# Kernel tuning notes

Hardware: AMD Instinct MI355X
Metric: run time of the kernel (lower is better)

## Reference

```python
import jax, jax.numpy as jnp
import numpy as np

DIM_EMB = 1024
NUM_HEADS = 16
DIM_HEAD = DIM_EMB // NUM_HEADS  # 64


def setup_inputs() -> dict:
    key = jax.random.key(0)
    k1, k2, k3 = jax.random.split(key, 3)
    x = jax.random.normal(k1, (4, 2048, DIM_EMB), dtype=jnp.float32)
    # nn.Linear(dim_embedding, 3*h*d, bias=False): weight shape [out, in]
    w_qkv = jax.random.normal(k2, (3 * NUM_HEADS * DIM_HEAD, DIM_EMB), dtype=jnp.float32) * (DIM_EMB ** -0.5)
    w_out = jax.random.normal(k3, (DIM_EMB, NUM_HEADS * DIM_HEAD), dtype=jnp.float32) * ((NUM_HEADS * DIM_HEAD) ** -0.5)
    return {"x": x, "w_qkv": w_qkv, "w_out": w_out}


def reference(x, w_qkv, w_out):
    b, t, _ = x.shape
    scale = DIM_HEAD ** -0.5
    qkv = jnp.einsum('bte,fe->btf', x, w_qkv)  # [b, t, 3*h*d]
    qkv = qkv.reshape(b, t, 3, NUM_HEADS, DIM_HEAD)  # fused dim order (k h d)
    q, k, v = qkv[:, :, 0], qkv[:, :, 1], qkv[:, :, 2]  # each [b, t, h, d]
    scores = jnp.einsum('bihd,bjhd->bhij', q, k) * scale  # [b, h, t, t]
    weights = jax.nn.softmax(scores, axis=-1)
    attn = jnp.einsum('bhij,bjhd->bhid', weights, v)  # [b, h, t, d]
    concat = attn.transpose(0, 2, 1, 3).reshape(b, t, NUM_HEADS * DIM_HEAD)
    return jnp.einsum('btf,ef->bte', concat, w_out)
```

## Files before the change

kernel.cpp:

```cpp
#include <hip/hip_runtime.h>

#define DI __device__ __forceinline__

typedef float  f32x2  __attribute__((ext_vector_type(2)));
typedef float  f32x4  __attribute__((ext_vector_type(4)));
typedef float  f32x16 __attribute__((ext_vector_type(16)));
typedef __bf16 bf16x8 __attribute__((ext_vector_type(8)));
typedef unsigned u32x2 __attribute__((ext_vector_type(2)));
typedef unsigned u32x4 __attribute__((ext_vector_type(4)));

static constexpr int TB   = 2048;
static constexpr int NTOK = 8192;
static constexpr int EMB  = 1024;
static constexpr int FQKV = 3072;

DI unsigned short f2bf(float f) {
  union { float f; unsigned u; } v; v.f = f;
  unsigned r = v.u + 0x7FFFu + ((v.u >> 16) & 1u);
  return (unsigned short)(r >> 16);
}

DI unsigned pack2bf(float a, float b) {
#if __has_builtin(__builtin_amdgcn_cvt_pk_bf16_f32)
  typedef __bf16 bf16x2 __attribute__((ext_vector_type(2)));
  bf16x2 r = __builtin_amdgcn_cvt_pk_bf16_f32(a, b);
  return __builtin_bit_cast(unsigned, r);
#else
  unsigned ua = __builtin_bit_cast(unsigned, a) + 0x8000u;
  unsigned ub = __builtin_bit_cast(unsigned, b) + 0x8000u;
  return __builtin_amdgcn_perm(ub, ua, 0x07060302u);
#endif
}

DI void plswap(unsigned& a, unsigned& b) {
#if __has_builtin(__builtin_amdgcn_permlane32_swap)
  u32x2 r = __builtin_amdgcn_permlane32_swap(a, b, false, false);
  a = r.x; b = r.y;
#else
  const bool hi = (threadIdx.x & 32) != 0;
  unsigned ax = (unsigned)__shfl_xor((int)a, 32);
  unsigned bx = (unsigned)__shfl_xor((int)b, 32);
  unsigned na = hi ? bx : a;
  unsigned nb = hi ? b : ax;
  a = na; b = nb;
#endif
}

DI bf16x8 frag4(unsigned a, unsigned b, unsigned c, unsigned d) {
  u32x4 u = {a, b, c, d};
  return __builtin_bit_cast(bf16x8, u);
}

DI void gload16(const void* g, void* l) {
  __builtin_amdgcn_global_load_lds(
      (__attribute__((address_space(1))) void*)(g),
      (__attribute__((address_space(3))) void*)(l), 16, 0, 0);
}

DI void syncdrain() {
  __builtin_amdgcn_s_waitcnt(0);
  __syncthreads();
}

__global__ __launch_bounds__(256)
void cvt_kernel(const float4* __restrict__ x, const float4* __restrict__ wq,
                const float4* __restrict__ wo,
                ushort4* __restrict__ xb, ushort4* __restrict__ wqb,
                ushort4* __restrict__ wob) {
  const int i  = blockIdx.x * 256 + threadIdx.x;
  const int nx = NTOK * EMB / 4;
  const int nq = FQKV * EMB / 4;
  float4 v; ushort4* dst;
  if (i < nx)           { v = x[i];           dst = xb  + i; }
  else if (i < nx + nq) { v = wq[i - nx];     dst = wqb + (i - nx); }
  else                  { v = wo[i - nx - nq]; dst = wob + (i - nx - nq); }
  ushort4 p;
  p.x = f2bf(v.x); p.y = f2bf(v.y); p.z = f2bf(v.z); p.w = f2bf(v.w);
  *dst = p;
}

template <int MODE>
__global__ __launch_bounds__(256)
void gemm_bt(const unsigned short* __restrict__ A,
             const unsigned short* __restrict__ Bt,
             const int K,
             unsigned short* __restrict__ qk,
             unsigned short* __restrict__ vT,
             float* __restrict__ outp) {
  __shared__ unsigned short sA[128 * 32];
  __shared__ unsigned short sB[128 * 32];
  const int tid  = threadIdx.x;
  const int w    = tid >> 6;
  const int l    = tid & 63;
  const int quad = l >> 4;
  const int lr   = l & 15;
  const int n0   = blockIdx.x * 128;
  const int m0   = blockIdx.y * 128;
  const int wm   = (w >> 1) * 64;
  const int wn   = (w & 1) * 64;

  f32x4 acc[4][4];
#pragma unroll
  for (int i = 0; i < 4; ++i)
#pragma unroll
    for (int j = 0; j < 4; ++j) acc[i][j] = {0.f, 0.f, 0.f, 0.f};

  const int srow = l >> 2;
  const int sg   = (l & 3) ^ ((l >> 3) & 3);
  const unsigned short* gA = A  + (long)(m0 + w * 32 + srow) * K + sg * 8;
  const unsigned short* gB = Bt + (long)(n0 + w * 32 + srow) * K + sg * 8;
  unsigned short* lA = sA + w * 1024;
  unsigned short* lB = sB + w * 1024;
  const int swz = (lr >> 1) & 3;

  for (int k0 = 0; k0 < K; k0 += 32) {
    gload16(gA + k0,          lA);
    gload16(gA + k0 + 16 * K, lA + 512);
    gload16(gB + k0,          lB);
    gload16(gB + k0 + 16 * K, lB + 512);
    syncdrain();
    bf16x8 af[4], bfr[4];
#pragma unroll
    for (int rt = 0; rt < 4; ++rt)
      af[rt] = *(const bf16x8*)(sA + (wm + rt * 16 + lr) * 32 + (quad ^ swz) * 8);
#pragma unroll
    for (int ct = 0; ct < 4; ++ct)
      bfr[ct] = *(const bf16x8*)(sB + (wn + ct * 16 + lr) * 32 + (quad ^ swz) * 8);
#pragma unroll
    for (int rt = 0; rt < 4; ++rt)
#pragma unroll
      for (int ct = 0; ct < 4; ++ct)
        acc[rt][ct] = __builtin_amdgcn_mfma_f32_16x16x32_bf16(af[rt], bfr[ct],
                                                              acc[rt][ct], 0, 0, 0);
    __syncthreads();
  }

  if (MODE == 0) {
    if (n0 < 2048) {
      const float qs = (n0 < 1024) ? 0.18033688011112042f : 1.0f;
#pragma unroll
      for (int rt = 0; rt < 4; ++rt) {
        const int row = m0 + wm + rt * 16 + quad * 4;
#pragma unroll
        for (int ct = 0; ct < 4; ++ct) {
          const int col = n0 + wn + ct * 16 + lr;
#pragma unroll
          for (int r = 0; r < 4; ++r)
            qk[(long)(row + r) * 2048 + col] = f2bf(acc[rt][ct][r] * qs);
        }
      }
    } else {
#pragma unroll
      for (int rt = 0; rt < 4; ++rt) {
        const int tok = m0 + wm + rt * 16 + quad * 4;
        const int bb  = tok >> 11, tt = tok & 2047;
#pragma unroll
        for (int ct = 0; ct < 4; ++ct) {
          const int fv = n0 - 2048 + wn + ct * 16 + lr;
          ushort4 p;
          p.x = f2bf(acc[rt][ct][0]); p.y = f2bf(acc[rt][ct][1]);
          p.z = f2bf(acc[rt][ct][2]); p.w = f2bf(acc[rt][ct][3]);
          *(ushort4*)(vT + ((long)(bb * 1024 + fv)) * 2048 + tt) = p;
        }
      }
    }
  } else {
#pragma unroll
    for (int rt = 0; rt < 4; ++rt) {
      const int row = m0 + wm + rt * 16 + quad * 4;
#pragma unroll
      for (int ct = 0; ct < 4; ++ct) {
        const int col = n0 + wn + ct * 16 + lr;
#pragma unroll
        for (int r = 0; r < 4; ++r)
          outp[(long)(row + r) * 1024 + col] = acc[rt][ct][r];
      }
    }
  }
}

__global__ __launch_bounds__(256, 4)
void attn_kernel(const unsigned short* __restrict__ qk,
                 const unsigned short* __restrict__ vT,
                 unsigned short* __restrict__ attnb) {
  __shared__ unsigned short sK[2][64 * 64];
  __shared__ unsigned short sV[2][64 * 64];
  const int tid = threadIdx.x;
  const int w   = tid >> 6;
  const int l   = tid & 63;
  const int l31 = l & 31;
  const int lh  = l >> 5;
  const int h8  = lh * 8;
  const int bh  = blockIdx.x;
  const int hh  = bh & 15;
  const long tokbase = (long)(bh >> 4) * TB;
  const int qbase = blockIdx.y * 128 + w * 32;

  bf16x8 qf[4];
  {
    const unsigned short* qptr = qk + (tokbase + qbase + l31) * 2048 + hh * 64 + h8;
#pragma unroll
    for (int s = 0; s < 4; ++s) qf[s] = *(const bf16x8*)(qptr + s * 16);
  }

  const int srow = l >> 3;
  const int g    = (l & 7) ^ srow;
  const unsigned short* kbase =
      qk + (tokbase + w * 16 + srow) * 2048 + 1024 + hh * 64 + g * 8;
  const unsigned short* vbase =
      vT + ((long)bh * 64 + w * 16 + srow) * 2048 + g * 8;

  f32x16 oacc[2] = {{}, {}};
  f32x2 lp2 = {0.f, 0.f};

  gload16(kbase,            &sK[0][(w * 16 + 0) * 64]);
  gload16(kbase + 8 * 2048, &sK[0][(w * 16 + 8) * 64]);
  gload16(vbase,            &sV[0][(w * 16 + 0) * 64]);
  gload16(vbase + 8 * 2048, &sV[0][(w * 16 + 8) * 64]);
  syncdrain();

  for (int t = 0; t < 32; ++t) {
    const int buf = t & 1;
    if (t + 1 < 32) {
      const int k0 = (t + 1) * 64;
      const int nb = buf ^ 1;
      gload16(kbase + (long)k0 * 2048,            &sK[nb][(w * 16 + 0) * 64]);
      gload16(kbase + (long)k0 * 2048 + 8 * 2048, &sK[nb][(w * 16 + 8) * 64]);
      gload16(vbase + k0,                         &sV[nb][(w * 16 + 0) * 64]);
      gload16(vbase + k0 + 8 * 2048,              &sV[nb][(w * 16 + 8) * 64]);
    }
    const unsigned short* bK = sK[buf];
    const unsigned short* bV = sV[buf];

#pragma unroll
    for (int G = 0; G < 2; ++G) {
      f32x16 sacc = {};
      __builtin_amdgcn_s_setprio(1);
#pragma unroll
      for (int s = 0; s < 4; ++s) {
        const int key = G * 32 + l31;
        const int p   = (s * 2 + lh) ^ (key & 7);
        const bf16x8 kf = *(const bf16x8*)(bK + key * 64 + p * 8);
        sacc = __builtin_amdgcn_mfma_f32_32x32x16_bf16(kf, qf[s], sacc, 0, 0, 0);
      }
      __builtin_amdgcn_s_setprio(0);
      float e[16];
#pragma unroll
      for (int i = 0; i < 16; ++i) e[i] = __builtin_amdgcn_exp2f(sacc[i]);
#pragma unroll
      for (int i = 0; i < 8; ++i) {
        f32x2 pr = {e[2 * i], e[2 * i + 1]};
        lp2 += pr;
      }
      unsigned d[8];
#pragma unroll
      for (int i = 0; i < 8; ++i) d[i] = pack2bf(e[2 * i], e[2 * i + 1]);
      plswap(d[0], d[2]); plswap(d[1], d[3]);
      plswap(d[4], d[6]); plswap(d[5], d[7]);
      bf16x8 pp[2];
      pp[0] = frag4(d[0], d[1], d[2], d[3]);
      pp[1] = frag4(d[4], d[5], d[6], d[7]);
      __builtin_amdgcn_s_setprio(1);
#pragma unroll
      for (int sub = 0; sub < 2; ++sub) {
        const int gt  = (G * 2 + sub) * 2 + lh;
        const int d0r = l31, d1r = 32 + l31;
        const bf16x8 vf0 = *(const bf16x8*)(bV + d0r * 64 + ((gt ^ (d0r & 7))) * 8);
        const bf16x8 vf1 = *(const bf16x8*)(bV + d1r * 64 + ((gt ^ (d1r & 7))) * 8);
        oacc[0] = __builtin_amdgcn_mfma_f32_32x32x16_bf16(pp[sub], vf0, oacc[0], 0, 0, 0);
        oacc[1] = __builtin_amdgcn_mfma_f32_32x32x16_bf16(pp[sub], vf1, oacc[1], 0, 0, 0);
      }
      __builtin_amdgcn_s_setprio(0);
    }
    syncdrain();
  }

  const float lp = lp2.x + lp2.y;
  const float fs = lp + __shfl_xor(lp, 32);
  const float rc = 1.0f / fs;
#pragma unroll
  for (int r = 0; r < 16; ++r) {
    const int row = (r & 3) + 8 * (r >> 2) + 4 * lh;
    const float sc = __shfl(rc, row);
    const long base = (tokbase + qbase + row) * 1024 + hh * 64;
    attnb[base + l31]      = f2bf(oacc[0][r] * sc);
    attnb[base + 32 + l31] = f2bf(oacc[1][r] * sc);
  }
}

extern "C" void kernel_launch(void* const* d_in, const int* in_sizes, int n_in,
                              void* d_out, int out_size, void* d_ws, size_t ws_size,
                              hipStream_t stream) {
  const float* x    = (const float*)d_in[0];
  const float* wqkv = (const float*)d_in[1];
  const float* wout = (const float*)d_in[2];
  float* outp = (float*)d_out;

  unsigned short* xb    = (unsigned short*)d_ws;
  unsigned short* wqkvb = xb    + (long)NTOK * EMB;
  unsigned short* woutb = wqkvb + (long)FQKV * EMB;
  unsigned short* qkb   = woutb + (long)EMB * EMB;
  unsigned short* vTb   = qkb   + (long)NTOK * 2048;
  unsigned short* attnb = vTb   + (long)4 * 16 * 64 * TB;

  cvt_kernel<<<12288, 256, 0, stream>>>(
      (const float4*)x, (const float4*)wqkv, (const float4*)wout,
      (ushort4*)xb, (ushort4*)wqkvb, (ushort4*)woutb);

  gemm_bt<0><<<dim3(24, 64), 256, 0, stream>>>(xb, wqkvb, EMB, qkb, vTb, nullptr);

  attn_kernel<<<dim3(64, 16), 256, 0, stream>>>(qkb, vTb, attnb);

  gemm_bt<1><<<dim3(8, 64), 256, 0, stream>>>(attnb, woutb, EMB, nullptr, nullptr, outp);
}
```

Measured before the change: 274.2 us.

## Use 256x256 double-buffered QKV GEMM and double-buffer output GEMM with block swizzle

Replaces the 128x128 QKV projection GEMM with a new 512-thread kernel using 256x256 tiles, a K-step of 64, double-buffered LDS and an XOR-swizzled layout. The generic GEMM also gets double-buffered LDS so global loads for the next K-tile overlap MFMA work on the current one. Both GEMMs remap block indices so neighbouring workgroups share input tiles in cache. The larger tile raises data reuse and cuts LDS traffic per flop, at the cost of heavy register and LDS use (128 KB LDS per block), which limits occupancy.

Measured after the change: 276.5 us. Within noise of the previous version (+0.8%).

```diff
diff --git a/kernel.cpp b/kernel.cpp
--- a/kernel.cpp
+++ b/kernel.cpp
@@ -79,6 +79,109 @@
   *dst = p;
 }
 
+__global__ __launch_bounds__(512, 2)
+void gemm256(const unsigned short* __restrict__ A,
+             const unsigned short* __restrict__ Bt,
+             const int K,
+             unsigned short* __restrict__ qk,
+             unsigned short* __restrict__ vT) {
+  __shared__ unsigned short sA[2][256 * 64];
+  __shared__ unsigned short sB[2][256 * 64];
+  const int tid  = threadIdx.x;
+  const int w    = tid >> 6;
+  const int l    = tid & 63;
+  const int quad = l >> 4;
+  const int lr   = l & 15;
+  const int nwg  = gridDim.x * gridDim.y;
+  const int orig = blockIdx.y * gridDim.x + blockIdx.x;
+  const int swz  = (orig & 7) * (nwg >> 3) + (orig >> 3);
+  const int n0   = (swz % gridDim.x) * 256;
+  const int m0   = (swz / gridDim.x) * 256;
+  const int wm   = (w >> 2) * 128;
+  const int wn   = (w & 3) * 64;
+
+  f32x4 acc[8][4];
+#pragma unroll
+  for (int i = 0; i < 8; ++i)
+#pragma unroll
+    for (int j = 0; j < 4; ++j) acc[i][j] = {0.f, 0.f, 0.f, 0.f};
+
+  const int srow8 = l >> 3;
+  const int gsw   = ((l & 7) ^ srow8) * 8;
+  const unsigned short* gA0 = A  + (long)(m0 + w * 8 + srow8) * K + gsw;
+  const unsigned short* gB0 = Bt + (long)(n0 + w * 8 + srow8) * K + gsw;
+
+  const int NT = K >> 6;
+
+#define STAGE256(buf, kk)                                                      \
+  do {                                                                         \
+    _Pragma("unroll")                                                          \
+    for (int jj = 0; jj < 4; ++jj) {                                           \
+      gload16(gA0 + (long)jj * 64 * K + (kk), &sA[buf][(jj * 64 + w * 8) * 64]);\
+      gload16(gB0 + (long)jj * 64 * K + (kk), &sB[buf][(jj * 64 + w * 8) * 64]);\
+    }                                                                          \
+  } while (0)
+
+  STAGE256(0, 0);
+  syncdrain();
+
+  for (int t = 0; t < NT; ++t) {
+    const int cur = t & 1;
+    if (t + 1 < NT) STAGE256(cur ^ 1, (t + 1) * 64);
+    const unsigned short* aS = &sA[cur][0];
+    const unsigned short* bS = &sB[cur][0];
+#pragma unroll
+    for (int ks = 0; ks < 2; ++ks) {
+      bf16x8 bfr[4];
+#pragma unroll
+      for (int nf = 0; nf < 4; ++nf) {
+        const int r = wn + nf * 16 + lr;
+        bfr[nf] = *(const bf16x8*)(bS + r * 64 + ((ks * 4 + quad) ^ (r & 7)) * 8);
+      }
+#pragma unroll
+      for (int m = 0; m < 8; ++m) {
+        const int ra = wm + m * 16 + lr;
+        const bf16x8 af = *(const bf16x8*)(aS + ra * 64 + ((ks * 4 + quad) ^ (ra & 7)) * 8);
+#pragma unroll
+        for (int nf = 0; nf < 4; ++nf)
+          acc[m][nf] = __builtin_amdgcn_mfma_f32_16x16x32_bf16(af, bfr[nf],
+                                                               acc[m][nf], 0, 0, 0);
+      }
+    }
+    syncdrain();
+  }
+#undef STAGE256
+
+  if (n0 < 2048) {
+    const float qs = (n0 < 1024) ? 0.18033688011112042f : 1.0f;
+#pragma unroll
+    for (int m = 0; m < 8; ++m) {
+      const int row = m0 + wm + m * 16 + quad * 4;
+#pragma unroll
+      for (int nf = 0; nf < 4; ++nf) {
+        const int col = n0 + wn + nf * 16 + lr;
+#pragma unroll
+        for (int r = 0; r < 4; ++r)
+          qk[(long)(row + r) * 2048 + col] = f2bf(acc[m][nf][r] * qs);
+      }
+    }
+  } else {
+#pragma unroll
+    for (int m = 0; m < 8; ++m) {
+      const int tok = m0 + wm + m * 16 + quad * 4;
+      const int bb  = tok >> 11, tt = tok & 2047;
+#pragma unroll
+      for (int nf = 0; nf < 4; ++nf) {
+        const int fv = n0 - 2048 + wn + nf * 16 + lr;
+        ushort4 p;
+        p.x = f2bf(acc[m][nf][0]); p.y = f2bf(acc[m][nf][1]);
+        p.z = f2bf(acc[m][nf][2]); p.w = f2bf(acc[m][nf][3]);
+        *(ushort4*)(vT + ((long)(bb * 1024 + fv)) * 2048 + tt) = p;
+      }
+    }
+  }
+}
+
 template <int MODE>
 __global__ __launch_bounds__(256)
 void gemm_bt(const unsigned short* __restrict__ A,
@@ -87,15 +190,18 @@
              unsigned short* __restrict__ qk,
              unsigned short* __restrict__ vT,
              float* __restrict__ outp) {
-  __shared__ unsigned short sA[128 * 32];
-  __shared__ unsigned short sB[128 * 32];
+  __shared__ unsigned short sA[2][128 * 32];
+  __shared__ unsigned short sB[2][128 * 32];
   const int tid  = threadIdx.x;
   const int w    = tid >> 6;
   const int l    = tid & 63;
   const int quad = l >> 4;
   const int lr   = l & 15;
-  const int n0   = blockIdx.x * 128;
-  const int m0   = blockIdx.y * 128;
+  const int nwg  = gridDim.x * gridDim.y;
+  const int orig = blockIdx.y * gridDim.x + blockIdx.x;
+  const int swzb = (orig & 7) * (nwg >> 3) + (orig >> 3);
+  const int n0   = (swzb % gridDim.x) * 128;
+  const int m0   = (swzb / gridDim.x) * 128;
   const int wm   = (w >> 1) * 64;
   const int wn   = (w & 1) * 64;
 
@@ -109,30 +215,39 @@
   const int sg   = (l & 3) ^ ((l >> 3) & 3);
   const unsigned short* gA = A  + (long)(m0 + w * 32 + srow) * K + sg * 8;
   const unsigned short* gB = Bt + (long)(n0 + w * 32 + srow) * K + sg * 8;
-  unsigned short* lA = sA + w * 1024;
-  unsigned short* lB = sB + w * 1024;
-  const int swz = (lr >> 1) & 3;
-
-  for (int k0 = 0; k0 < K; k0 += 32) {
-    gload16(gA + k0,          lA);
-    gload16(gA + k0 + 16 * K, lA + 512);
-    gload16(gB + k0,          lB);
-    gload16(gB + k0 + 16 * K, lB + 512);
-    syncdrain();
+  const int lofs = w * 1024;
+  const int swz  = (lr >> 1) & 3;
+  const int NT   = K >> 5;
+
+  gload16(gA,          &sA[0][lofs]);
+  gload16(gA + 16 * K, &sA[0][lofs + 512]);
+  gload16(gB,          &sB[0][lofs]);
+  gload16(gB + 16 * K, &sB[0][lofs + 512]);
+  syncdrain();
+
+  for (int t = 0; t < NT; ++t) {
+    const int cur = t & 1;
+    if (t + 1 < NT) {
+      const int k0 = (t + 1) * 32;
+      gload16(gA + k0,          &sA[cur ^ 1][lofs]);
+      gload16(gA + k0 + 16 * K, &sA[cur ^ 1][lofs + 512]);
+      gload16(gB + k0,          &sB[cur ^ 1][lofs]);
+      gload16(gB + k0 + 16 * K, &sB[cur ^ 1][lofs + 512]);
+    }
     bf16x8 af[4], bfr[4];
 #pragma unroll
     for (int rt = 0; rt < 4; ++rt)
-      af[rt] = *(const bf16x8*)(sA + (wm + rt * 16 + lr) * 32 + (quad ^ swz) * 8);
+      af[rt] = *(const bf16x8*)(&sA[cur][(wm + rt * 16 + lr) * 32 + (quad ^ swz) * 8]);
 #pragma unroll
     for (int ct = 0; ct < 4; ++ct)
-      bfr[ct] = *(const bf16x8*)(sB + (wn + ct * 16 + lr) * 32 + (quad ^ swz) * 8);
+      bfr[ct] = *(const bf16x8*)(&sB[cur][(wn + ct * 16 + lr) * 32 + (quad ^ swz) * 8]);
 #pragma unroll
     for (int rt = 0; rt < 4; ++rt)
 #pragma unroll
       for (int ct = 0; ct < 4; ++ct)
         acc[rt][ct] = __builtin_amdgcn_mfma_f32_16x16x32_bf16(af[rt], bfr[ct],
                                                               acc[rt][ct], 0, 0, 0);
-    __syncthreads();
+    syncdrain();
   }
 
   if (MODE == 0) {
@@ -307,7 +422,7 @@
       (const float4*)x, (const float4*)wqkv, (const float4*)wout,
       (ushort4*)xb, (ushort4*)wqkvb, (ushort4*)woutb);
 
-  gemm_bt<0><<<dim3(24, 64), 256, 0, stream>>>(xb, wqkvb, EMB, qkb, vTb, nullptr);
+  gemm256<<<dim3(12, 32), 512, 0, stream>>>(xb, wqkvb, EMB, qkb, vTb);
 
   attn_kernel<<<dim3(64, 16), 256, 0, stream>>>(qkb, vTb, attnb);
 
```

## Replace GEMMs with 256x256 double-buffered 8-wave pipelined kernel; relax attention waits

Applied to the files above, without the earlier changes.

The QKV and output-projection GEMMs now use a 256x256 tile with 8 waves, a K-step of 64 and double-buffered LDS. Global-to-LDS loads are staged across four compute phases with counted vmcnt waits instead of a full drain each iteration. A block-index swizzle is added to improve L2 locality. The attention kernel replaces its full waitcnt(0)+syncthreads with vmcnt(4) waits and raw barriers so the next tile's prefetch can stay in flight. The risks are lower occupancy from the larger LDS footprint, fewer workgroups for the output GEMM (128 blocks), and correctness depending on the hand-counted waits.

New measurement: 287.6 us. +4.9%, slower.

```diff
diff --git a/kernel.cpp b/kernel.cpp
--- a/kernel.cpp
+++ b/kernel.cpp
@@ -56,6 +56,11 @@
       (__attribute__((address_space(1))) void*)(g),
       (__attribute__((address_space(3))) void*)(l), 16, 0, 0);
 }
+
+DI void wait_vm4() { asm volatile("s_waitcnt vmcnt(4)" ::: "memory"); }
+DI void wait_vm0() { asm volatile("s_waitcnt vmcnt(0)" ::: "memory"); }
+DI void rbar()     { __builtin_amdgcn_s_barrier(); }
+DI void sfence()   { __builtin_amdgcn_sched_barrier(0); }
 
 DI void syncdrain() {
   __builtin_amdgcn_s_waitcnt(0);
@@ -80,100 +85,169 @@
 }
 
 template <int MODE>
-__global__ __launch_bounds__(256)
-void gemm_bt(const unsigned short* __restrict__ A,
-             const unsigned short* __restrict__ Bt,
-             const int K,
-             unsigned short* __restrict__ qk,
-             unsigned short* __restrict__ vT,
-             float* __restrict__ outp) {
-  __shared__ unsigned short sA[128 * 32];
-  __shared__ unsigned short sB[128 * 32];
+__global__ __launch_bounds__(512, 2)
+void gemm8p(const unsigned short* __restrict__ A,
+            const unsigned short* __restrict__ Bt,
+            const int K,
+            unsigned short* __restrict__ qk,
+            unsigned short* __restrict__ vT,
+            float* __restrict__ outp) {
+  __shared__ unsigned short sA[2][256 * 64];
+  __shared__ unsigned short sB[2][256 * 64];
   const int tid  = threadIdx.x;
   const int w    = tid >> 6;
   const int l    = tid & 63;
   const int quad = l >> 4;
   const int lr   = l & 15;
-  const int n0   = blockIdx.x * 128;
-  const int m0   = blockIdx.y * 128;
-  const int wm   = (w >> 1) * 64;
-  const int wn   = (w & 1) * 64;
-
-  f32x4 acc[4][4];
-#pragma unroll
-  for (int i = 0; i < 4; ++i)
+  const int nwg  = gridDim.x * gridDim.y;
+  const int orig = blockIdx.y * gridDim.x + blockIdx.x;
+  const int swz  = (orig & 7) * (nwg >> 3) + (orig >> 3);
+  const int n0   = (swz % gridDim.x) * 256;
+  const int m0   = (swz / gridDim.x) * 256;
+  const int wm   = (w >> 2) * 128;
+  const int wn   = (w & 3) * 64;
+
+  f32x4 acc[8][4];
+#pragma unroll
+  for (int i = 0; i < 8; ++i)
 #pragma unroll
     for (int j = 0; j < 4; ++j) acc[i][j] = {0.f, 0.f, 0.f, 0.f};
 
-  const int srow = l >> 2;
-  const int sg   = (l & 3) ^ ((l >> 3) & 3);
-  const unsigned short* gA = A  + (long)(m0 + w * 32 + srow) * K + sg * 8;
-  const unsigned short* gB = Bt + (long)(n0 + w * 32 + srow) * K + sg * 8;
-  unsigned short* lA = sA + w * 1024;
-  unsigned short* lB = sB + w * 1024;
-  const int swz = (lr >> 1) & 3;
-
-  for (int k0 = 0; k0 < K; k0 += 32) {
-    gload16(gA + k0,          lA);
-    gload16(gA + k0 + 16 * K, lA + 512);
-    gload16(gB + k0,          lB);
-    gload16(gB + k0 + 16 * K, lB + 512);
-    syncdrain();
-    bf16x8 af[4], bfr[4];
-#pragma unroll
-    for (int rt = 0; rt < 4; ++rt)
-      af[rt] = *(const bf16x8*)(sA + (wm + rt * 16 + lr) * 32 + (quad ^ swz) * 8);
-#pragma unroll
-    for (int ct = 0; ct < 4; ++ct)
-      bfr[ct] = *(const bf16x8*)(sB + (wn + ct * 16 + lr) * 32 + (quad ^ swz) * 8);
-#pragma unroll
-    for (int rt = 0; rt < 4; ++rt)
-#pragma unroll
-      for (int ct = 0; ct < 4; ++ct)
-        acc[rt][ct] = __builtin_amdgcn_mfma_f32_16x16x32_bf16(af[rt], bfr[ct],
-                                                              acc[rt][ct], 0, 0, 0);
-    __syncthreads();
-  }
+  const int srow8 = l >> 3;
+  const int gsw   = ((l & 7) ^ srow8) * 8;
+  int rA[2][2], rB[2][2];
+#pragma unroll
+  for (int mh = 0; mh < 2; ++mh)
+#pragma unroll
+    for (int jj = 0; jj < 2; ++jj) {
+      const int q0 = w * 16 + jj * 8;
+      rA[mh][jj] = ((q0 >> 6) << 7) + mh * 64 + (q0 & 63);
+      rB[mh][jj] = ((q0 >> 5) << 6) + mh * 32 + (q0 & 31);
+    }
+  const unsigned short* gAp[2][2];
+  const unsigned short* gBp[2][2];
+  int ldsA[2][2], ldsB[2][2];
+#pragma unroll
+  for (int mh = 0; mh < 2; ++mh)
+#pragma unroll
+    for (int jj = 0; jj < 2; ++jj) {
+      gAp[mh][jj] = A  + (long)(m0 + rA[mh][jj] + srow8) * K + gsw;
+      gBp[mh][jj] = Bt + (long)(n0 + rB[mh][jj] + srow8) * K + gsw;
+      ldsA[mh][jj] = rA[mh][jj] * 64;
+      ldsB[mh][jj] = rB[mh][jj] * 64;
+    }
+
+  const int NT = K >> 6;
+
+#define SG_A(buf, t, mh)                                                \
+  do {                                                                  \
+    gload16(gAp[mh][0] + (t) * 64, &sA[buf][ldsA[mh][0]]);              \
+    gload16(gAp[mh][1] + (t) * 64, &sA[buf][ldsA[mh][1]]);              \
+  } while (0)
+#define SG_B(buf, t, nh)                                                \
+  do {                                                                  \
+    gload16(gBp[nh][0] + (t) * 64, &sB[buf][ldsB[nh][0]]);              \
+    gload16(gBp[nh][1] + (t) * 64, &sB[buf][ldsB[nh][1]]);              \
+  } while (0)
+
+  SG_A(0, 0, 0); SG_B(0, 0, 0); SG_A(0, 0, 1); SG_B(0, 0, 1);
+  SG_A(1, 1, 0); SG_B(1, 1, 0);
+  sfence(); wait_vm4(); sfence();
+  rbar();
+
+  for (int t = 0; t < NT; ++t) {
+    const int cur = t & 1;
+    const int nxt = cur ^ 1;
+    const unsigned short* aS = &sA[cur][0];
+    const unsigned short* bS = &sB[cur][0];
+
+#define PHASE(mh, nh, STG, BOUND)                                            \
+    do {                                                                     \
+      bf16x8 afr[4][2], bfr[2][2];                                           \
+      _Pragma("unroll")                                                      \
+      for (int ks = 0; ks < 2; ++ks) {                                       \
+        _Pragma("unroll")                                                    \
+        for (int nf = 0; nf < 2; ++nf) {                                     \
+          const int r = wn + (nh) * 32 + nf * 16 + lr;                       \
+          bfr[nf][ks] = *(const bf16x8*)(bS + r * 64 +                       \
+                          (((ks * 4 + quad) ^ (r & 7)) * 8));                \
+        }                                                                    \
+        _Pragma("unroll")                                                    \
+        for (int m = 0; m < 4; ++m) {                                        \
+          const int r = wm + (mh) * 64 + m * 16 + lr;                        \
+          afr[m][ks] = *(const bf16x8*)(aS + r * 64 +                        \
+                          (((ks * 4 + quad) ^ (r & 7)) * 8));                \
+        }                                                                    \
+      }                                                                      \
+      STG;                                                                   \
+      __builtin_amdgcn_s_setprio(1);                                         \
+      _Pragma("unroll")                                                      \
+      for (int m = 0; m < 4; ++m)                                            \
+        _Pragma("unroll")                                                    \
+        for (int nf = 0; nf < 2; ++nf)                                       \
+          _Pragma("unroll")                                                  \
+          for (int ks = 0; ks < 2; ++ks)                                     \
+            acc[(mh) * 4 + m][(nh) * 2 + nf] =                               \
+                __builtin_amdgcn_mfma_f32_16x16x32_bf16(                     \
+                    afr[m][ks], bfr[nf][ks],                                 \
+                    acc[(mh) * 4 + m][(nh) * 2 + nf], 0, 0, 0);              \
+      __builtin_amdgcn_s_setprio(0);                                         \
+      if (BOUND) {                                                           \
+        sfence();                                                            \
+        if (t + 2 < NT) wait_vm4(); else wait_vm0();                         \
+        sfence();                                                            \
+      }                                                                      \
+      rbar();                                                                \
+    } while (0)
+
+    PHASE(0, 0, if (t + 1 < NT) SG_A(nxt, t + 1, 1), false);
+    PHASE(0, 1, if (t + 1 < NT) SG_B(nxt, t + 1, 1), false);
+    PHASE(1, 0, if (t + 2 < NT) SG_A(cur, t + 2, 0), false);
+    PHASE(1, 1, if (t + 2 < NT) SG_B(cur, t + 2, 0), (t + 1 < NT));
+#undef PHASE
+  }
+#undef SG_A
+#undef SG_B
 
   if (MODE == 0) {
     if (n0 < 2048) {
       const float qs = (n0 < 1024) ? 0.18033688011112042f : 1.0f;
 #pragma unroll
-      for (int rt = 0; rt < 4; ++rt) {
-        const int row = m0 + wm + rt * 16 + quad * 4;
-#pragma unroll
-        for (int ct = 0; ct < 4; ++ct) {
-          const int col = n0 + wn + ct * 16 + lr;
+      for (int m = 0; m < 8; ++m) {
+        const int row = m0 + wm + m * 16 + quad * 4;
+#pragma unroll
+        for (int nf = 0; nf < 4; ++nf) {
+          const int col = n0 + wn + nf * 16 + lr;
 #pragma unroll
           for (int r = 0; r < 4; ++r)
-            qk[(long)(row + r) * 2048 + col] = f2bf(acc[rt][ct][r] * qs);
+            qk[(long)(row + r) * 2048 + col] = f2bf(acc[m][nf][r] * qs);
         }
       }
     } else {
 #pragma unroll
-      for (int rt = 0; rt < 4; ++rt) {
-        const int tok = m0 + wm + rt * 16 + quad * 4;
+      for (int m = 0; m < 8; ++m) {
+        const int tok = m0 + wm + m * 16 + quad * 4;
         const int bb  = tok >> 11, tt = tok & 2047;
 #pragma unroll
-        for (int ct = 0; ct < 4; ++ct) {
-          const int fv = n0 - 2048 + wn + ct * 16 + lr;
+        for (int nf = 0; nf < 4; ++nf) {
+          const int fv = n0 - 2048 + wn + nf * 16 + lr;
           ushort4 p;
-          p.x = f2bf(acc[rt][ct][0]); p.y = f2bf(acc[rt][ct][1]);
-          p.z = f2bf(acc[rt][ct][2]); p.w = f2bf(acc[rt][ct][3]);
+          p.x = f2bf(acc[m][nf][0]); p.y = f2bf(acc[m][nf][1]);
+          p.z = f2bf(acc[m][nf][2]); p.w = f2bf(acc[m][nf][3]);
           *(ushort4*)(vT + ((long)(bb * 1024 + fv)) * 2048 + tt) = p;
         }
       }
     }
   } else {
 #pragma unroll
-    for (int rt = 0; rt < 4; ++rt) {
-      const int row = m0 + wm + rt * 16 + quad * 4;
-#pragma unroll
-      for (int ct = 0; ct < 4; ++ct) {
-        const int col = n0 + wn + ct * 16 + lr;
+    for (int m = 0; m < 8; ++m) {
+      const int row = m0 + wm + m * 16 + quad * 4;
+#pragma unroll
+      for (int nf = 0; nf < 4; ++nf) {
+        const int col = n0 + wn + nf * 16 + lr;
 #pragma unroll
         for (int r = 0; r < 4; ++r)
-          outp[(long)(row + r) * 1024 + col] = acc[rt][ct][r];
+          outp[(long)(row + r) * 1024 + col] = acc[m][nf][r];
       }
     }
   }
@@ -217,7 +291,6 @@
   gload16(kbase + 8 * 2048, &sK[0][(w * 16 + 8) * 64]);
   gload16(vbase,            &sV[0][(w * 16 + 0) * 64]);
   gload16(vbase + 8 * 2048, &sV[0][(w * 16 + 8) * 64]);
-  syncdrain();
 
   for (int t = 0; t < 32; ++t) {
     const int buf = t & 1;
@@ -228,7 +301,13 @@
       gload16(kbase + (long)k0 * 2048 + 8 * 2048, &sK[nb][(w * 16 + 8) * 64]);
       gload16(vbase + k0,                         &sV[nb][(w * 16 + 0) * 64]);
       gload16(vbase + k0 + 8 * 2048,              &sV[nb][(w * 16 + 8) * 64]);
-    }
+      wait_vm4();
+    } else {
+      wait_vm0();
+    }
+    sfence();
+    rbar();
+    sfence();
     const unsigned short* bK = sK[buf];
     const unsigned short* bV = sV[buf];
 
@@ -272,7 +351,8 @@
       }
       __builtin_amdgcn_s_setprio(0);
     }
-    syncdrain();
+    sfence();
+    rbar();
   }
 
   const float lp = lp2.x + lp2.y;
@@ -307,9 +387,9 @@
       (const float4*)x, (const float4*)wqkv, (const float4*)wout,
       (ushort4*)xb, (ushort4*)wqkvb, (ushort4*)woutb);
 
-  gemm_bt<0><<<dim3(24, 64), 256, 0, stream>>>(xb, wqkvb, EMB, qkb, vTb, nullptr);
+  gemm8p<0><<<dim3(12, 32), 512, 0, stream>>>(xb, wqkvb, EMB, qkb, vTb, nullptr);
 
   attn_kernel<<<dim3(64, 16), 256, 0, stream>>>(qkb, vTb, attnb);
 
-  gemm_bt<1><<<dim3(8, 64), 256, 0, stream>>>(attnb, woutb, EMB, nullptr, nullptr, outp);
-}
+  gemm8p<1><<<dim3(4, 32), 512, 0, stream>>>(attnb, woutb, EMB, nullptr, nullptr, outp);
+}
```
